# Performance work log

Measured on AMD Instinct MI355X. Metric: run time of the kernel, lower is better.

Reference implementation:

```python
import jax, jax.numpy as jnp
import numpy as np
import math

N_LEVELS = 16
F_PER = 2
LOG2T = 19
TABLE = 1 << LOG2T  # 524288
BASE = 16
FINEST = 512
BANDS = 10
TIME = 0.0

_B = math.exp((math.log(FINEST) - math.log(BASE)) / (N_LEVELS - 1))
_RES = [min(int(BASE * _B ** l), FINEST) for l in range(N_LEVELS)]
# primes reduced mod table size: (c*p) mod M == (c*(p mod M)) mod M, keeps products in int32 range
_PRIMES_MOD = np.array([73856093 % TABLE, 19349663 % TABLE, 83492791 % TABLE], dtype=np.int32)
_OFFSETS = np.array([[dx, dy, dz] for dx in (0, 1) for dy in (0, 1) for dz in (0, 1)], dtype=bool)  # [8,3]


def _hash_encode(x, tables):
    # x: [N,3] in [0,1]; tables: [L, 2^19, 2]
    x = jnp.clip(x, 0.0, 1.0)
    offs = jnp.asarray(_OFFSETS)[:, None, :]  # [8,1,3]
    pm = jnp.asarray(_PRIMES_MOD)
    outs = []
    for l in range(N_LEVELS):
        res = _RES[l]
        sc = x * (res - 1)                                   # [N,3]
        cf = jnp.clip(jnp.floor(sc).astype(jnp.int32), 0, res - 1)
        cc = jnp.clip(cf + 1, 0, res - 1)
        w = sc - cf.astype(sc.dtype)                         # trilinear weights [N,3]
        corner = jnp.where(offs, cc[None], cf[None])         # [8,N,3]
        h = ((corner[..., 0] * pm[0]) % TABLE
             + (corner[..., 1] * pm[1]) % TABLE
             + (corner[..., 2] * pm[2]) % TABLE) % TABLE     # [8,N]
        feats = tables[l][h]                                 # gather [8,N,2]
        cw = jnp.prod(jnp.where(offs, w[None], 1.0 - w[None]), axis=-1)  # [8,N]
        outs.append(jnp.sum(feats * cw[..., None], axis=0))  # [N,2]
    return jnp.concatenate(outs, axis=1)                     # [N,32]


def _freq_encode(freq):
    nf = (jnp.log10(jnp.clip(freq, 1e6, 1e12)) - 6.0) / 6.0  # [N,1]
    parts = []
    for i in range(BANDS):
        a = (2.0 ** i) * math.pi * nf
        parts += [jnp.sin(a), jnp.cos(a)]
    return jnp.concatenate(parts, axis=-1)                   # [N,20]


def _ln(x, g, b, eps=1e-5):
    m = jnp.mean(x, -1, keepdims=True)
    v = jnp.var(x, -1, keepdims=True)
    return (x - m) / jnp.sqrt(v + eps) * g + b


def _forward(x, frequency, tables, W0, b0, W1, b1, W2, b2, W3, b3,
             e_w1, e_b1, e_g, e_be, e_w2, e_b2,
             m_w1, m_b1, m_g, m_be, m_w2, m_b2,
             p_w1, p_b1, p_w2, p_b2,
             mat_w1, mat_b1, mat_w2, mat_b2,
             s_w1, s_b1, s_w2, s_b2):
    pe = _hash_encode(x, tables)                             # [N,32]
    fe = _freq_encode(frequency)                             # [N,20]
    feat0 = jnp.concatenate([pe, fe], axis=1)                # [N,52]
    h = jax.nn.relu(feat0 @ W0 + b0)
    h = jax.nn.relu(h @ W1 + b1)
    h = jax.nn.relu(jnp.concatenate([h, feat0], axis=1) @ W2 + b2)  # skip connection
    h = jax.nn.relu(h @ W3 + b3)
    E_amp = jnp.tanh(jax.nn.relu(_ln(h @ e_w1 + e_b1, e_g, e_be)) @ e_w2 + e_b2)
    B_amp = jnp.tanh(jax.nn.relu(_ln(h @ m_w1 + m_b1, m_g, m_be)) @ m_w2 + m_b2)
    phases = jax.nn.relu(h @ p_w1 + p_b1) @ p_w2 + p_b2      # [N,6]
    mat = jax.nn.relu(h @ mat_w1 + mat_b1) @ mat_w2 + mat_b2 # [N,3]
    src = jax.nn.relu(h @ s_w1 + s_b1) @ s_w2 + s_b2         # [N,4]
    omega = 2.0 * math.pi * frequency                        # [N,1]
    E = E_amp * jnp.cos(omega * TIME + phases[:, :3])
    B = B_amp * jnp.cos(omega * TIME + phases[:, 3:])
    eps_r = 1.0 + jax.nn.sigmoid(mat[:, 0:1]) * 10.0
    mu_r = 1.0 + jax.nn.sigmoid(mat[:, 1:2]) * 2.0
    cond = jax.nn.sigmoid(mat[:, 2:3]) * 0.01
    # pack all float outputs: E(3) B(3) eps(1) mu(1) cond(1) charge(1) current(3)
    return jnp.concatenate([E, B, eps_r, mu_r, cond, src[:, 0:1], src[:, 1:4]], axis=1)


def _lin_init(k, fan_in, fan_out):
    k1, k2 = jax.random.split(k)
    s = 1.0 / math.sqrt(fan_in)
    W = jax.random.uniform(k1, (fan_in, fan_out), jnp.float32, -s, s)
    b = jax.random.uniform(k2, (fan_out,), jnp.float32, -s, s)
    return W, b


def setup_inputs() -> dict:
    key = jax.random.key(0)
    ks = jax.random.split(key, 20)
    N = 262144
    d = {}
    d['x'] = jax.random.uniform(ks[0], (N, 3), jnp.float32)
    d['frequency'] = 10.0 ** jax.random.uniform(ks[1], (N, 1), jnp.float32, minval=6.0, maxval=12.0)
    d['tables'] = jax.random.normal(ks[2], (N_LEVELS, TABLE, F_PER), jnp.float32) * 1e-4
    layers = [('W0', 'b0', 52, 128), ('W1', 'b1', 128, 128), ('W2', 'b2', 180, 128), ('W3', 'b3', 128, 128),
              ('e_w1', 'e_b1', 128, 64), ('e_w2', 'e_b2', 64, 3),
              ('m_w1', 'm_b1', 128, 64), ('m_w2', 'm_b2', 64, 3),
              ('p_w1', 'p_b1', 128, 32), ('p_w2', 'p_b2', 32, 6),
              ('mat_w1', 'mat_b1', 128, 64), ('mat_w2', 'mat_b2', 64, 3),
              ('s_w1', 's_b1', 128, 64), ('s_w2', 's_b2', 64, 4)]
    for j, (wn, bn, fi, fo) in enumerate(layers):
        W, b = _lin_init(jax.random.fold_in(ks[3], j), fi, fo)
        d[wn] = W
        d[bn] = b
    d['e_g'] = jnp.ones(64, jnp.float32)
    d['e_be'] = jnp.zeros(64, jnp.float32)
    d['m_g'] = jnp.ones(64, jnp.float32)
    d['m_be'] = jnp.zeros(64, jnp.float32)
    return d


def reference(x, frequency, tables, W0, b0, W1, b1, W2, b2, W3, b3,
              e_w1, e_b1, e_g, e_be, e_w2, e_b2,
              m_w1, m_b1, m_g, m_be, m_w2, m_b2,
              p_w1, p_b1, p_w2, p_b2,
              mat_w1, mat_b1, mat_w2, mat_b2,
              s_w1, s_b1, s_w2, s_b2):
    return _forward(x, frequency, tables, W0, b0, W1, b1, W2, b2, W3, b3,
                    e_w1, e_b1, e_g, e_be, e_w2, e_b2,
                    m_w1, m_b1, m_g, m_be, m_w2, m_b2,
                    p_w1, p_b1, p_w2, p_b2,
                    mat_w1, mat_b1, mat_w2, mat_b2,
                    s_w1, s_b1, s_w2, s_b2)
```

## Files before the change

kernel.cpp:

```cpp
#include <hip/hip_runtime.h>
#include <math.h>

#define TMASK 524287
#define PM0 455773
#define PM1 475295
#define PM2 130999

typedef __attribute__((ext_vector_type(8))) short bf16x8;
typedef __attribute__((ext_vector_type(4))) float f32x4;

#define OFF_W0   0
#define OFF_W1   8192
#define OFF_W2   24576
#define OFF_W3   49152
#define OFF_E    65536
#define OFF_P    81920
#define OFF_MAT  86016
#define OFF_S    94208
#define OFF_BD   102400
#define WT_TOTAL 102400
#define WT_ALLOC 111616

#define WS_TAB8_OFF (WT_ALLOC*2)
#define TAB8_BYTES  (16u*524288u*2u)
#define WS_FEAT_OFF (WS_TAB8_OFF + TAB8_BYTES)
#define DENSE_BYTES 120992

#define TAB_SCALE   131072.0f
#define TAB_INV     (1.0f/131072.0f)

#define A6_H    0
#define A6_HL   8704
#define A6_FB   8704
#define LDS6_TOTAL 17408

struct Params {
  const float* x; const float* freq; const float* tables;
  const float* b0; const float* b1; const float* b2; const float* b3;
  const float* e_b1; const float* e_w2; const float* e_b2; const float* e_g; const float* e_be;
  const float* m_b1; const float* m_w2; const float* m_b2; const float* m_g; const float* m_be;
  const float* p_b1; const float* p_w2; const float* p_b2;
  const float* mat_b1; const float* mat_w2; const float* mat_b2;
  const float* s_b1; const float* s_w2; const float* s_b2;
  const short* wt;
  const unsigned* feat;
  const unsigned short* dense;
  float* out;
  int N;
  int res[16];
};

struct HashParams {
  const float* x; const unsigned short* tab8; unsigned* feat; int N; int res[16];
};
struct DensePrepParams { const unsigned short* tab8; unsigned short* dense; };
struct TabPrepParams { const float* tables; unsigned* tab8; };
struct PrepParams {
  const float* src[9];
  int end[9]; int Nsrc[9]; int Ksrc[9]; int Kpad[9];
  short* wt;
};
struct BdParams {
  const float* e; const float* m; const float* p; const float* mat; const float* s;
  short* out;
};

__device__ __forceinline__ short f2bf(float f){
  union { float f; unsigned u; } v; v.f = f;
  unsigned r = v.u + 0x7fffu + ((v.u >> 16) & 1u);
  return (short)(r >> 16);
}
__device__ __forceinline__ float bf2f(short s){
  union { unsigned u; float f; } v; v.u = ((unsigned)(unsigned short)s) << 16; return v.f;
}
__device__ __forceinline__ float sigmoid_(float v){ return 1.f/(1.f + expf(-v)); }

__global__ __launch_bounds__(256)
void prep_weights(PrepParams P)
{
  int id = blockIdx.x*256 + threadIdx.x;
  if (id >= WT_TOTAL) return;
  int r = 0, base = 0;
  #pragma unroll
  for (int i = 0; i < 9; ++i) { if (id >= P.end[i]) { r = i+1; base = P.end[i]; } }
  const int rel = id - base;
  const int kp = P.Kpad[r];
  const int n = rel / kp;
  const int k = rel - n*kp;
  float v = 0.f;
  if (k < P.Ksrc[r]) v = P.src[r][k * P.Nsrc[r] + n];
  P.wt[id] = f2bf(v);
}

__global__ __launch_bounds__(256)
void prep_bd(BdParams P)
{
  int id = blockIdx.x*256 + threadIdx.x;
  if (id >= 32*288) return;
  const int n = id / 288, k = id - n*288;
  float v = 0.f;
  if      (n < 3  && k < 64)                        v = P.e[k*3 + n];
  else if (n >= 3 && n < 6  && k >= 64  && k < 128) v = P.m[(k-64)*3 + (n-3)];
  else if (n >= 6 && n < 12 && k >= 256)            v = P.p[(k-256)*6 + (n-6)];
  else if (n >= 12&& n < 15 && k >= 128 && k < 192) v = P.mat[(k-128)*3 + (n-12)];
  else if (n >= 15&& n < 19 && k >= 192 && k < 256) v = P.s[(k-192)*4 + (n-15)];
  P.out[id] = f2bf(v);
}

__global__ __launch_bounds__(256)
void tab_prep(TabPrepParams P)
{
  const unsigned id = blockIdx.x*256 + threadIdx.x;
  if (id >= 16u*524288u/2u) return;
  const float4 v = ((const float4*)P.tables)[id];
  int q0 = (int)fminf(fmaxf(rintf(v.x*TAB_SCALE), -127.f), 127.f);
  int q1 = (int)fminf(fmaxf(rintf(v.y*TAB_SCALE), -127.f), 127.f);
  int q2 = (int)fminf(fmaxf(rintf(v.z*TAB_SCALE), -127.f), 127.f);
  int q3 = (int)fminf(fmaxf(rintf(v.w*TAB_SCALE), -127.f), 127.f);
  unsigned pack = (q0 & 255) | ((q1 & 255) << 8) | ((q2 & 255) << 16) | ((q3 & 255) << 24);
  P.tab8[id] = pack;
}

__global__ __launch_bounds__(256)
void dense_prep(DensePrepParams P)
{
  const int id = blockIdx.x*256 + threadIdx.x;
  const int l = id >> 15;
  const int c = id & 32767;
  const int RT4[4] = {16,20,25,32};
  const unsigned DOFFU[4] = {0, 4096, 12096, 27728};
  const int res = RT4[l];
  if (c >= res*res*res) return;
  const int cz = c % res;
  const int t  = c / res;
  const int cy = t % res;
  const int cx = t / res;
  const unsigned h = (unsigned)((cx*PM0 + cy*PM1 + cz*PM2) & TMASK);
  P.dense[DOFFU[l] + c] = P.tab8[((unsigned)l << 19) + h];
}

__global__ __launch_bounds__(256, 8)
void hash_encode12(HashParams P)
{
  const int b = blockIdx.x;
  const int unit = b % 24;
  const int strip = b / 24;
  const int l = 4 + (unit >> 1);
  const int half = unit & 1;
  const int halfN = (P.N + 1) >> 1;
  const int plA = strip*512 + threadIdx.x;
  if (plA >= halfN) return;
  const int plB = plA + 256;
  const bool vB = plB < halfN;
  int pA = half*halfN + plA;
  int pB = half*halfN + (vB ? plB : plA);
  const bool sA = pA < P.N;
  const bool sB = vB && (pB < P.N);
  if (pA >= P.N) pA = P.N - 1;
  if (pB >= P.N) pB = P.N - 1;

  const int res = P.res[l];
  const float rf = (float)(res-1);
  const unsigned short* tp = P.tab8 + ((size_t)l << 19);

  const float xA0 = fminf(fmaxf(P.x[pA*3+0], 0.f), 1.f);
  const float xA1 = fminf(fmaxf(P.x[pA*3+1], 0.f), 1.f);
  const float xA2 = fminf(fmaxf(P.x[pA*3+2], 0.f), 1.f);
  const float sA0 = xA0*rf, sA1 = xA1*rf, sA2 = xA2*rf;
  int fA0 = (int)sA0; if (fA0 > res-1) fA0 = res-1;
  int fA1 = (int)sA1; if (fA1 > res-1) fA1 = res-1;
  int fA2 = (int)sA2; if (fA2 > res-1) fA2 = res-1;
  const float wA0 = sA0 - (float)fA0;
  const float wA1 = sA1 - (float)fA1;
  const float wA2 = sA2 - (float)fA2;
  int cA0 = fA0+1; if (cA0 > res-1) cA0 = res-1;
  int cA1 = fA1+1; if (cA1 > res-1) cA1 = res-1;
  int cA2 = fA2+1; if (cA2 > res-1) cA2 = res-1;
  const int hxA0 = (fA0*PM0) & TMASK, hxA1 = (cA0*PM0) & TMASK;
  const int hyA0 = (fA1*PM1) & TMASK, hyA1 = (cA1*PM1) & TMASK;
  const int hzA0 = (fA2*PM2) & TMASK, hzA1 = (cA2*PM2) & TMASK;

  const float xB0 = fminf(fmaxf(P.x[pB*3+0], 0.f), 1.f);
  const float xB1 = fminf(fmaxf(P.x[pB*3+1], 0.f), 1.f);
  const float xB2 = fminf(fmaxf(P.x[pB*3+2], 0.f), 1.f);
  const float sB0 = xB0*rf, sB1 = xB1*rf, sB2 = xB2*rf;
  int fB0 = (int)sB0; if (fB0 > res-1) fB0 = res-1;
  int fB1 = (int)sB1; if (fB1 > res-1) fB1 = res-1;
  int fB2 = (int)sB2; if (fB2 > res-1) fB2 = res-1;
  const float wB0 = sB0 - (float)fB0;
  const float wB1 = sB1 - (float)fB1;
  const float wB2 = sB2 - (float)fB2;
  int cB0 = fB0+1; if (cB0 > res-1) cB0 = res-1;
  int cB1 = fB1+1; if (cB1 > res-1) cB1 = res-1;
  int cB2 = fB2+1; if (cB2 > res-1) cB2 = res-1;
  const int hxB0 = (fB0*PM0) & TMASK, hxB1 = (cB0*PM0) & TMASK;
  const int hyB0 = (fB1*PM1) & TMASK, hyB1 = (cB1*PM1) & TMASK;
  const int hzB0 = (fB2*PM2) & TMASK, hzB1 = (cB2*PM2) & TMASK;

  unsigned short tvA[8], tvB[8];
  #pragma unroll
  for (int cn = 0; cn < 8; ++cn) {
    const int bx = (cn>>2)&1, by = (cn>>1)&1, bz = cn&1;
    tvA[cn] = tp[((bx?hxA1:hxA0) + (by?hyA1:hyA0) + (bz?hzA1:hzA0)) & TMASK];
    tvB[cn] = tp[((bx?hxB1:hxB0) + (by?hyB1:hyB0) + (bz?hzB1:hzB0)) & TMASK];
  }

  unsigned* fl = P.feat + (size_t)(l-4)*P.N;
  {
    float a0 = 0.f, a1 = 0.f;
    #pragma unroll
    for (int cn = 0; cn < 8; ++cn) {
      const int bx = (cn>>2)&1, by = (cn>>1)&1, bz = cn&1;
      const float cw = (bx?wA0:1.f-wA0)*(by?wA1:1.f-wA1)*(bz?wA2:1.f-wA2);
      a0 = fmaf(cw, (float)(int)(signed char)(tvA[cn] & 0xff), a0);
      a1 = fmaf(cw, (float)(int)(signed char)(tvA[cn] >> 8),   a1);
    }
    a0 *= TAB_INV; a1 *= TAB_INV;
    if (sA)
      fl[pA] = (unsigned)(unsigned short)f2bf(a0)
             | ((unsigned)(unsigned short)f2bf(a1) << 16);
  }
  {
    float a0 = 0.f, a1 = 0.f;
    #pragma unroll
    for (int cn = 0; cn < 8; ++cn) {
      const int bx = (cn>>2)&1, by = (cn>>1)&1, bz = cn&1;
      const float cw = (bx?wB0:1.f-wB0)*(by?wB1:1.f-wB1)*(bz?wB2:1.f-wB2);
      a0 = fmaf(cw, (float)(int)(signed char)(tvB[cn] & 0xff), a0);
      a1 = fmaf(cw, (float)(int)(signed char)(tvB[cn] >> 8),   a1);
    }
    a0 *= TAB_INV; a1 *= TAB_INV;
    if (sB)
      fl[pB] = (unsigned)(unsigned short)f2bf(a0)
             | ((unsigned)(unsigned short)f2bf(a1) << 16);
  }
}

template<int NT, int KC>
__device__ __forceinline__ void gemm32(f32x4* acc0, f32x4* acc1,
    const short* A, int lda, const short* __restrict__ wt, int kpad, int kwoff,
    int n0, int q)
{
  const short* Ap0 = A + n0*lda + q*8;
  const short* Ap1 = Ap0 + 16*lda;
  const short* Bp  = wt + n0*kpad + kwoff + q*8;
  bf16x8 bc[NT], bn[NT];
  #pragma unroll
  for (int nt = 0; nt < NT; ++nt) bc[nt] = *(const bf16x8*)(Bp + nt*16*kpad);
  #pragma unroll
  for (int kc = 0; kc < KC; ++kc) {
    if (kc + 1 < KC) {
      #pragma unroll
      for (int nt = 0; nt < NT; ++nt)
        bn[nt] = *(const bf16x8*)(Bp + nt*16*kpad + (kc+1)*32);
    }
    const bf16x8 a0 = *(const bf16x8*)(Ap0 + kc*32);
    const bf16x8 a1 = *(const bf16x8*)(Ap1 + kc*32);
    #pragma unroll
    for (int nt = 0; nt < NT; ++nt) {
      acc0[nt] = __builtin_amdgcn_mfma_f32_16x16x32_bf16(a0, bc[nt], acc0[nt], 0, 0, 0);
      acc1[nt] = __builtin_amdgcn_mfma_f32_16x16x32_bf16(a1, bc[nt], acc1[nt], 0, 0, 0);
    }
    #pragma unroll
    for (int nt = 0; nt < NT; ++nt) bc[nt] = bn[nt];
  }
}

template<int NT>
__device__ __forceinline__ void epi_trunk(const f32x4* acc0, const f32x4* acc1,
    const float* bv4, short* out, int ldo, int n0, int q, int coff)
{
  #pragma unroll
  for (int nt = 0; nt < NT; ++nt) {
    const float bv = bv4[nt];
    #pragma unroll
    for (int r = 0; r < 4; ++r) {
      float v0 = fmaxf(acc0[nt][r] + bv, 0.f);
      float v1 = fmaxf(acc1[nt][r] + bv, 0.f);
      out[(q*4 + r)*ldo + coff + nt*16 + n0]      = f2bf(v0);
      out[(16 + q*4 + r)*ldo + coff + nt*16 + n0] = f2bf(v1);
    }
  }
}

__global__ __launch_bounds__(128, 4)
void em_nerf6(Params P)
{
  __shared__ __align__(16) char smem[LDS6_TOTAL];
  const int tid = threadIdx.x;
  const int lane = tid & 63, wave = tid >> 6;
  short* H  = (short*)(smem + A6_H);
  short* HL = (short*)(smem + A6_HL);
  short* FB = (short*)(smem + A6_FB);
  float* R2 = (float*)(smem + A6_HL);
  const int n0 = lane & 15, q = lane >> 4;
  const int p0 = blockIdx.x*32;
  const int ntb = wave*64;

  const int pp = tid & 31;
  const int lg = tid >> 5;

  unsigned fw3[3];
  {
    int gp = p0 + pp; if (gp >= P.N) gp = P.N - 1;
    #pragma unroll
    for (int j = 0; j < 3; ++j)
      fw3[j] = P.feat[(size_t)(lg*3 + j)*P.N + gp];
  }

  float rb0[4], rb1[4], rb2[4], rb3[4], rbem[4], rbms[4], rg[4], rbe[4];
  {
    const float* embp = wave ? P.m_b1 : P.e_b1;
    const float* msbp = wave ? P.s_b1 : P.mat_b1;
    const float* ggp  = wave ? P.m_g  : P.e_g;
    const float* bbep = wave ? P.m_be : P.e_be;
    #pragma unroll
    for (int nt = 0; nt < 4; ++nt) {
      const int c  = ntb + nt*16 + n0;
      const int ch = nt*16 + n0;
      rb0[nt] = P.b0[c]; rb1[nt] = P.b1[c]; rb2[nt] = P.b2[c]; rb3[nt] = P.b3[c];
      rbem[nt] = embp[ch]; rbms[nt] = msbp[ch];
      rg[nt] = ggp[ch]; rbe[nt] = bbep[ch];
    }
  }
  const float rpb = P.p_b1[wave*16 + n0];
  float rc;
  if (wave == 0) {
    if      (n0 < 3)  rc = P.e_b2[n0];
    else if (n0 < 6)  rc = P.m_b2[n0-3];
    else if (n0 < 12) rc = P.p_b2[n0-6];
    else if (n0 < 15) rc = P.mat_b2[n0-12];
    else              rc = P.s_b2[0];
  } else {
    rc = (n0 < 3) ? P.s_b2[1 + n0] : 0.f;
  }

  unsigned short ctv[8];
  float cw0, cw1, cw2;
  {
    int gpc = p0 + pp; if (gpc >= P.N) gpc = P.N - 1;
    const float xs0 = fminf(fmaxf(P.x[gpc*3+0], 0.f), 1.f);
    const float xs1 = fminf(fmaxf(P.x[gpc*3+1], 0.f), 1.f);
    const float xs2 = fminf(fmaxf(P.x[gpc*3+2], 0.f), 1.f);
    const int lo  = (lg & 1) ? 20 : 16;
    const int hi  = (lg & 1) ? 32 : 25;
    const int res = (lg & 2) ? hi : lo;
    const unsigned dlo  = (lg & 1) ? 4096u  : 0u;
    const unsigned dhi  = (lg & 1) ? 27728u : 12096u;
    const unsigned doff = (lg & 2) ? dhi : dlo;
    const float rf = (float)(res-1);
    const float s0 = xs0*rf, s1 = xs1*rf, s2 = xs2*rf;
    int f0i = (int)s0; if (f0i > res-1) f0i = res-1;
    int f1i = (int)s1; if (f1i > res-1) f1i = res-1;
    int f2i = (int)s2; if (f2i > res-1) f2i = res-1;
    cw0 = s0 - (float)f0i;
    cw1 = s1 - (float)f1i;
    cw2 = s2 - (float)f2i;
    int c0i = f0i+1; if (c0i > res-1) c0i = res-1;
    int c1i = f1i+1; if (c1i > res-1) c1i = res-1;
    int c2i = f2i+1; if (c2i > res-1) c2i = res-1;
    const int sx0 = f0i*res*res, sx1 = c0i*res*res;
    const int ty0 = f1i*res,     ty1 = c1i*res;
    const unsigned short* dp = P.dense + doff;
    #pragma unroll
    for (int cn = 0; cn < 8; ++cn) {
      const int bx = (cn>>2)&1, by = (cn>>1)&1, bz = cn&1;
      const int idx = (bx?sx1:sx0) + (by?ty1:ty0) + (bz?c2i:f2i);
      ctv[cn] = dp[idx];
    }
  }

  {
    int gp = p0 + pp; if (gp >= P.N) gp = P.N - 1;
    float fr = P.freq[gp];
    fr = fminf(fmaxf(fr, 1e6f), 1e12f);
    const float nf = (log10f(fr) - 6.f) * (1.f/6.f);
    const float a0 = 3.14159274101257324f * nf;
    #pragma clang loop unroll(disable)
    for (int i = lg; i < 10; i += 4) {
      const float a = a0 * (float)(1 << i);
      FB[pp*72 + 32 + 2*i] = f2bf(sinf(a));
      FB[pp*72 + 33 + 2*i] = f2bf(cosf(a));
    }
    if (lg == 3) {
      #pragma unroll
      for (int k = 52; k < 64; ++k) FB[pp*72 + k] = 0;
    }
  }

  {
    float a0 = 0.f, a1 = 0.f;
    #pragma unroll
    for (int cn = 0; cn < 8; ++cn) {
      const int bx = (cn>>2)&1, by = (cn>>1)&1, bz = cn&1;
      const float cw = (bx?cw0:1.f-cw0)*(by?cw1:1.f-cw1)*(bz?cw2:1.f-cw2);
      a0 = fmaf(cw, (float)(int)(signed char)(ctv[cn] & 0xff), a0);
      a1 = fmaf(cw, (float)(int)(signed char)(ctv[cn] >> 8),   a1);
    }
    a0 *= TAB_INV; a1 *= TAB_INV;
    const unsigned pack = (unsigned)(unsigned short)f2bf(a0)
                        | ((unsigned)(unsigned short)f2bf(a1) << 16);
    *(unsigned*)&FB[pp*72 + 2*lg] = pack;
  }

  #pragma unroll
  for (int j = 0; j < 3; ++j)
    *(unsigned*)&FB[pp*72 + 8 + 2*(lg*3 + j)] = fw3[j];
  __syncthreads();

  { f32x4 a0[4] = {}, a1[4] = {};
    gemm32<4,2>(a0, a1, FB, 72, P.wt + OFF_W0 + ntb*64, 64, 0, n0, q);
    epi_trunk<4>(a0, a1, rb0, H, 136, n0, q, ntb);
    __syncthreads(); }
  { f32x4 a0[4] = {}, a1[4] = {};
    gemm32<4,4>(a0, a1, H, 136, P.wt + OFF_W1 + ntb*128, 128, 0, n0, q);
    __syncthreads();
    epi_trunk<4>(a0, a1, rb1, H, 136, n0, q, ntb);
    __syncthreads(); }
  { f32x4 a0[4] = {}, a1[4] = {};
    gemm32<4,4>(a0, a1, H, 136, P.wt + OFF_W2 + ntb*192, 192, 0, n0, q);
    gemm32<4,2>(a0, a1, FB, 72, P.wt + OFF_W2 + ntb*192, 192, 128, n0, q);
    __syncthreads();
    epi_trunk<4>(a0, a1, rb2, H, 136, n0, q, ntb);
    __syncthreads(); }
  { f32x4 a0[4] = {}, a1[4] = {};
    gemm32<4,4>(a0, a1, H, 136, P.wt + OFF_W3 + ntb*128, 128, 0, n0, q);
    __syncthreads();
    epi_trunk<4>(a0, a1, rb3, H, 136, n0, q, ntb);
    __syncthreads(); }

  { f32x4 a0[4] = {}, a1[4] = {};
    gemm32<4,4>(a0, a1, H, 136, P.wt + OFF_E + ntb*128, 128, 0, n0, q);
    #pragma unroll
    for (int nt = 0; nt < 4; ++nt) {
      const float bv = rbem[nt];
      #pragma unroll
      for (int r = 0; r < 4; ++r) { a0[nt][r] += bv; a1[nt][r] += bv; }
    }
    float mn[2][4], iv[2][4];
    #pragma unroll
    for (int s = 0; s < 2; ++s) {
      const f32x4* A_ = s ? a1 : a0;
      #pragma unroll
      for (int r = 0; r < 4; ++r) {
        float se = 0.f, qe = 0.f;
        #pragma unroll
        for (int t = 0; t < 4; ++t) { const float x = A_[t][r]; se += x; qe = fmaf(x,x,qe); }
        #pragma unroll
        for (int msk = 1; msk < 16; msk <<= 1) {
          se += __shfl_xor(se, msk, 64);
          qe += __shfl_xor(qe, msk, 64);
        }
        const float me = se*(1.f/64.f);
        mn[s][r] = me;
        iv[s][r] = 1.f / sqrtf(qe*(1.f/64.f) - me*me + 1e-5f);
      }
    }
    #pragma unroll
    for (int t = 0; t < 4; ++t) {
      const float g  = rg[t];
      const float be = rbe[t];
      const int col = ntb + t*16 + n0;
      #pragma unroll
      for (int s = 0; s < 2; ++s) {
        const f32x4* A_ = s ? a1 : a0;
        #pragma unroll
        for (int r = 0; r < 4; ++r) {
          float v = (A_[t][r] - mn[s][r])*iv[s][r]*g + be;
          v = fmaxf(v, 0.f);
          HL[(s*16 + q*4 + r)*136 + col] = f2bf(v);
        }
      }
    }
  }
  __syncthreads();

  f32x4 o0[1] = {}, o1[1] = {};
  gemm32<1,4>(o0, o1, HL, 136, P.wt + OFF_BD + wave*16*288, 288, 0, n0, q);

  { f32x4 a0[4] = {}, a1[4] = {};
    gemm32<4,4>(a0, a1, H, 136, P.wt + OFF_MAT + ntb*128, 128, 0, n0, q);
    __syncthreads();
    #pragma unroll
    for (int t = 0; t < 4; ++t) {
      const float bv = rbms[t];
      const int col = ntb + t*16 + n0;
      #pragma unroll
      for (int s = 0; s < 2; ++s) {
        const f32x4* A_ = s ? a1 : a0;
        #pragma unroll
        for (int r = 0; r < 4; ++r)
          HL[(s*16 + q*4 + r)*136 + col] = f2bf(fmaxf(A_[t][r] + bv, 0.f));
      }
    }
  }
  __syncthreads();

  gemm32<1,4>(o0, o1, HL, 136, P.wt + OFF_BD + wave*16*288, 288, 128, n0, q);

  { f32x4 a0[1] = {}, a1[1] = {};
    gemm32<1,4>(a0, a1, H, 136, P.wt + OFF_P + wave*16*128, 128, 0, n0, q);
    __syncthreads();
    const int col = wave*16 + n0;
    #pragma unroll
    for (int s = 0; s < 2; ++s) {
      const f32x4* A_ = s ? a1 : a0;
      #pragma unroll
      for (int r = 0; r < 4; ++r)
        HL[(s*16 + q*4 + r)*136 + col] = f2bf(fmaxf(A_[0][r] + rpb, 0.f));
    }
  }
  __syncthreads();

  gemm32<1,1>(o0, o1, HL, 136, P.wt + OFF_BD + wave*16*288, 288, 256, n0, q);
  __syncthreads();

  #pragma unroll
  for (int s = 0; s < 2; ++s) {
    const f32x4* O_ = s ? o1 : o0;
    #pragma unroll
    for (int r = 0; r < 4; ++r) {
      const int p = s*16 + q*4 + r;
      if (wave == 0) {
        float v0 = O_[0][r] + rc;
        if (n0 < 6) v0 = tanhf(v0);
        R2[p*20 + n0] = v0;
      } else if (n0 < 3) {
        R2[p*20 + 16 + n0] = O_[0][r] + rc;
      }
    }
  }
  __syncthreads();

  if (tid < 32) {
    const int gp = p0 + tid;
    if (gp < P.N) {
      const float* r = R2 + tid*20;
      float* o = P.out + (size_t)gp*13;
      o[0] = r[0]*cosf(r[6]);
      o[1] = r[1]*cosf(r[7]);
      o[2] = r[2]*cosf(r[8]);
      o[3] = r[3]*cosf(r[9]);
      o[4] = r[4]*cosf(r[10]);
      o[5] = r[5]*cosf(r[11]);
      o[6] = 1.f + sigmoid_(r[12])*10.f;
      o[7] = 1.f + sigmoid_(r[13])*2.f;
      o[8] = sigmoid_(r[14])*0.01f;
      o[9]  = r[15];
      o[10] = r[16];
      o[11] = r[17];
      o[12] = r[18];
    }
  }
}

__global__ __launch_bounds__(256, 3)
void em_nerf_fallback(Params P)
{
  __shared__ __align__(16) char smem[44288];
  short* featB = (short*)smem;
  short* hA    = (short*)(smem + 9216);
  short* hB    = (short*)(smem + 9216 + 17664);
  float* headF = (float*)(smem + 9216);
  float* res2  = (float*)smem;
  __shared__ int s_res[16];

  const int tid = threadIdx.x;
  if (tid < 16) s_res[tid] = P.res[tid];
  __syncthreads();
  {
    const int p = tid & 63;
    const int g = tid >> 6;
    int gp = blockIdx.x*64 + p; if (gp >= P.N) gp = P.N - 1;
    const float xs0 = fminf(fmaxf(P.x[gp*3+0], 0.f), 1.f);
    const float xs1 = fminf(fmaxf(P.x[gp*3+1], 0.f), 1.f);
    const float xs2 = fminf(fmaxf(P.x[gp*3+2], 0.f), 1.f);
    #pragma unroll
    for (int j = 0; j < 4; ++j) {
      const int l = g*4 + j;
      const int res = s_res[l];
      const float rf = (float)(res-1);
      const float s0 = xs0*rf, s1 = xs1*rf, s2 = xs2*rf;
      int f0i = (int)s0; if (f0i > res-1) f0i = res-1;
      int f1i = (int)s1; if (f1i > res-1) f1i = res-1;
      int f2i = (int)s2; if (f2i > res-1) f2i = res-1;
      const float w0 = s0 - (float)f0i;
      const float w1 = s1 - (float)f1i;
      const float w2 = s2 - (float)f2i;
      int c0i = f0i+1; if (c0i > res-1) c0i = res-1;
      int c1i = f1i+1; if (c1i > res-1) c1i = res-1;
      int c2i = f2i+1; if (c2i > res-1) c2i = res-1;
      const int hx0 = (f0i*PM0) & TMASK, hx1 = (c0i*PM0) & TMASK;
      const int hy0 = (f1i*PM1) & TMASK, hy1 = (c1i*PM1) & TMASK;
      const int hz0 = (f2i*PM2) & TMASK, hz1 = (c2i*PM2) & TMASK;
      const float* tp = P.tables + ((size_t)l << 20);
      float a0 = 0.f, a1 = 0.f;
      #pragma unroll
      for (int cn = 0; cn < 8; ++cn) {
        const int bx = (cn>>2)&1, by = (cn>>1)&1, bz = cn&1;
        const int hh = ((bx?hx1:hx0) + (by?hy1:hy0) + (bz?hz1:hz0)) & TMASK;
        const float cw = (bx?w0:1.f-w0)*(by?w1:1.f-w1)*(bz?w2:1.f-w2);
        const float2 tv = *(const float2*)(tp + 2*hh);
        a0 = fmaf(cw, tv.x, a0);
        a1 = fmaf(cw, tv.y, a1);
      }
      featB[p*72 + 2*l]   = f2bf(a0);
      featB[p*72 + 2*l+1] = f2bf(a1);
    }
    if (g == 0) {
      float fr = P.freq[gp];
      fr = fminf(fmaxf(fr, 1e6f), 1e12f);
      const float nf = (log10f(fr) - 6.f) * (1.f/6.f);
      float a = 3.14159274101257324f * nf;
      #pragma unroll
      for (int i = 0; i < 10; ++i) {
        featB[p*72 + 32 + 2*i] = f2bf(sinf(a));
        featB[p*72 + 33 + 2*i] = f2bf(cosf(a));
        a = a * 2.f;
      }
    }
    if (g == 3) {
      #pragma unroll
      for (int k = 52; k < 64; ++k) featB[p*72 + k] = 0;
    }
  }
  __syncthreads();

  const int lane = tid & 63, wave = tid >> 6;
  const int n0 = lane & 15, q = lane >> 4;
  short* myA  = featB + wave*16*72;
  short* myH1 = hA + wave*16*136;
  short* myH2 = hB + wave*16*136;

  auto gemm1 = [&](const short* A, int lda, const short* wt, int kpad, int kwoff, int KC, f32x4* acc, int NT){
    const short* Ap = A + n0*lda + q*8;
    const short* Bp = wt + n0*kpad + kwoff + q*8;
    for (int kc = 0; kc < KC; ++kc) {
      bf16x8 a = *(const bf16x8*)(Ap + kc*32);
      for (int nt = 0; nt < NT; ++nt) {
        bf16x8 b = *(const bf16x8*)(Bp + nt*16*kpad + kc*32);
        acc[nt] = __builtin_amdgcn_mfma_f32_16x16x32_bf16(a, b, acc[nt], 0, 0, 0);
      }
    }
  };
  auto epi1 = [&](const f32x4* acc, const float* bias, short* out, int ldo, int NT, bool relu){
    for (int nt = 0; nt < NT; ++nt) {
      const float bv = bias[nt*16 + n0];
      for (int r = 0; r < 4; ++r) {
        float v = acc[nt][r] + bv;
        if (relu) v = fmaxf(v, 0.f);
        out[(q*4 + r)*ldo + nt*16 + n0] = f2bf(v);
      }
    }
  };

  { f32x4 acc[8] = {}; gemm1(myA, 72, P.wt + OFF_W0, 64, 0, 2, acc, 8);  epi1(acc, P.b0, myH1, 136, 8, true); }
  __syncthreads();
  { f32x4 acc[8] = {}; gemm1(myH1, 136, P.wt + OFF_W1, 128, 0, 4, acc, 8); epi1(acc, P.b1, myH2, 136, 8, true); }
  __syncthreads();
  { f32x4 acc[8] = {}; gemm1(myH2, 136, P.wt + OFF_W2, 192, 0, 4, acc, 8);
    gemm1(myA, 72, P.wt + OFF_W2, 192, 128, 2, acc, 8); epi1(acc, P.b2, myH1, 136, 8, true); }
  __syncthreads();
  { f32x4 acc[8] = {}; gemm1(myH1, 136, P.wt + OFF_W3, 128, 0, 4, acc, 8); epi1(acc, P.b3, myH2, 136, 8, true); }
  __syncthreads();

  float* hf = headF + wave*16*69;
  auto head1f = [&](const short* wt, const float* bias, int NT, bool relu){
    f32x4 acc[4] = {};
    gemm1(myH2, 136, wt, 128, 0, 4, acc, NT);
    for (int nt = 0; nt < NT; ++nt) {
      const float bv = bias[nt*16 + n0];
      for (int r = 0; r < 4; ++r) {
        float v = acc[nt][r] + bv;
        if (relu) v = fmaxf(v, 0.f);
        hf[(q*4 + r)*69 + nt*16 + n0] = v;
      }
    }
  };
  auto l2 = [&](int OC2, int K2, bool ln, bool th, const float* g, const float* be,
                const float* W2, const float* b2, int slot){
    __syncthreads();
    if (tid < 64) {
      const float* row = headF + tid*69;
      float mn = 0.f, iv = 1.f;
      if (ln) {
        float s = 0.f;
        for (int k = 0; k < K2; ++k) s += row[k];
        mn = s/(float)K2;
        float vv = 0.f;
        for (int k = 0; k < K2; ++k) { float d = row[k]-mn; vv = fmaf(d,d,vv); }
        iv = 1.f/sqrtf(vv/(float)K2 + 1e-5f);
      }
      for (int j = 0; j < OC2; ++j) {
        float acc = b2[j];
        for (int k = 0; k < K2; ++k) {
          float xv = row[k];
          if (ln) xv = (xv-mn)*iv*g[k] + be[k];
          xv = fmaxf(xv, 0.f);
          acc = fmaf(xv, W2[k*OC2+j], acc);
        }
        res2[tid*20 + slot + j] = th ? tanhf(acc) : acc;
      }
    }
    __syncthreads();
  };

  head1f(P.wt + OFF_E, P.e_b1, 4, false); l2(3, 64, true,  true,  P.e_g, P.e_be, P.e_w2, P.e_b2, 0);
  head1f(P.wt + OFF_E + 8192, P.m_b1, 4, false); l2(3, 64, true, true, P.m_g, P.m_be, P.m_w2, P.m_b2, 3);
  head1f(P.wt + OFF_P, P.p_b1, 2, true);  l2(6, 32, false, false, 0, 0, P.p_w2, P.p_b2, 6);
  head1f(P.wt + OFF_MAT, P.mat_b1, 4, true); l2(3, 64, false, false, 0, 0, P.mat_w2, P.mat_b2, 12);
  head1f(P.wt + OFF_S, P.s_b1, 4, true);  l2(4, 64, false, false, 0, 0, P.s_w2, P.s_b2, 15);

  if (tid < 64) {
    const int gp = blockIdx.x*64 + tid;
    if (gp < P.N) {
      const float* r = res2 + tid*20;
      float* o = P.out + (size_t)gp*13;
      o[0] = r[0]*cosf(r[6]);
      o[1] = r[1]*cosf(r[7]);
      o[2] = r[2]*cosf(r[8]);
      o[3] = r[3]*cosf(r[9]);
      o[4] = r[4]*cosf(r[10]);
      o[5] = r[5]*cosf(r[11]);
      o[6] = 1.f + sigmoid_(r[12])*10.f;
      o[7] = 1.f + sigmoid_(r[13])*2.f;
      o[8] = sigmoid_(r[14])*0.01f;
      o[9]  = r[15];
      o[10] = r[16];
      o[11] = r[17];
      o[12] = r[18];
    }
  }
}

extern "C" void kernel_launch(void* const* d_in, const int* in_sizes, int n_in,
                              void* d_out, int out_size, void* d_ws, size_t ws_size,
                              hipStream_t stream) {
  (void)n_in; (void)out_size;
  const float** in = (const float**)d_in;
  const int N = in_sizes[0] / 3;

  PrepParams PP;
  const float* srcs[9] = { in[3], in[5], in[7], in[9], in[11], in[15], in[19], in[23], in[27] };
  const int ends[9]  = { 8192, 24576, 49152, 65536, 73728, 81920, 86016, 94208, 102400 };
  const int nsrc[9]  = { 128, 128, 128, 128, 64, 64, 32, 64, 64 };
  const int ksrc[9]  = { 52, 128, 180, 128, 128, 128, 128, 128, 128 };
  const int kpad[9]  = { 64, 128, 192, 128, 128, 128, 128, 128, 128 };
  for (int i = 0; i < 9; ++i) { PP.src[i]=srcs[i]; PP.end[i]=ends[i]; PP.Nsrc[i]=nsrc[i]; PP.Ksrc[i]=ksrc[i]; PP.Kpad[i]=kpad[i]; }
  PP.wt = (short*)d_ws;
  hipLaunchKernelGGL(prep_weights, dim3((WT_TOTAL+255)/256), dim3(256), 0, stream, PP);

  BdParams BP;
  BP.e = in[13]; BP.m = in[17]; BP.p = in[21]; BP.mat = in[25]; BP.s = in[29];
  BP.out = (short*)d_ws + OFF_BD;
  hipLaunchKernelGGL(prep_bd, dim3((32*288 + 255)/256), dim3(256), 0, stream, BP);

  Params P;
  P.x = in[0]; P.freq = in[1]; P.tables = in[2];
  P.b0 = in[4]; P.b1 = in[6]; P.b2 = in[8]; P.b3 = in[10];
  P.e_b1 = in[12]; P.e_w2 = in[13]; P.e_b2 = in[14];
  P.m_b1 = in[16]; P.m_w2 = in[17]; P.m_b2 = in[18];
  P.p_b1 = in[20]; P.p_w2 = in[21]; P.p_b2 = in[22];
  P.mat_b1 = in[24]; P.mat_w2 = in[25]; P.mat_b2 = in[26];
  P.s_b1 = in[28]; P.s_w2 = in[29]; P.s_b2 = in[30];
  P.e_g = in[31]; P.e_be = in[32]; P.m_g = in[33]; P.m_be = in[34];
  P.wt = (const short*)d_ws;
  P.feat = (const unsigned*)((const char*)d_ws + WS_FEAT_OFF);
  P.out = (float*)d_out;
  P.N = N;

  const double B = exp((log(512.0) - log(16.0)) / 15.0);
  for (int l = 0; l < 16; ++l) {
    double r = 16.0 * pow(B, (double)l);
    int ri = (int)r;
    if (ri > 512) ri = 512;
    P.res[l] = ri;
  }

  const size_t feat_bytes = (size_t)N*12*4;
  const size_t need = (size_t)WS_FEAT_OFF + feat_bytes + DENSE_BYTES;

  if (ws_size >= need) {
    char* dense_base = (char*)d_ws + WS_FEAT_OFF + feat_bytes;
    P.dense = (const unsigned short*)dense_base;

    TabPrepParams TP;
    TP.tables = in[2];
    TP.tab8 = (unsigned*)((char*)d_ws + WS_TAB8_OFF);
    hipLaunchKernelGGL(tab_prep, dim3((16*524288/2 + 255)/256), dim3(256), 0, stream, TP);

    DensePrepParams DP;
    DP.tab8 = (const unsigned short*)((const char*)d_ws + WS_TAB8_OFF);
    DP.dense = (unsigned short*)dense_base;
    hipLaunchKernelGGL(dense_prep, dim3(4*32768/256), dim3(256), 0, stream, DP);

    HashParams HP;
    HP.x = in[0];
    HP.tab8 = (const unsigned short*)((const char*)d_ws + WS_TAB8_OFF);
    HP.feat = (unsigned*)((char*)d_ws + WS_FEAT_OFF);
    HP.N = N;
    for (int l = 0; l < 16; ++l) HP.res[l] = P.res[l];
    const int halfN = (N + 1) >> 1;
    const int strips = (halfN + 511) / 512;
    hipLaunchKernelGGL(hash_encode12, dim3(strips*24), dim3(256), 0, stream, HP);

    hipLaunchKernelGGL(em_nerf6, dim3((N + 31) / 32), dim3(128), 0, stream, P);
  } else {
    P.dense = nullptr;
    hipLaunchKernelGGL(em_nerf_fallback, dim3((N + 63) / 64), dim3(256), 0, stream, P);
  }
}
```

Baseline: 491.1 us.

## Extend dense-grid precompute to levels 4-7 and blend them in main kernel

Levels 4-7 get a dense pre-gathered grid, the same treatment levels 0-3 already had, so their lookups index a compact array instead of the scattered hash table. The main kernel now computes these mid levels inline, and the separate hash kernel handles only levels 8-15. This shrinks the intermediate feature buffer and the hash kernel's work. In exchange, the dense prep kernel must gather about a million entries per call, and the main kernel takes on eight more gathers per point.

After: 471.2 us. 1.04x faster.

```diff
diff --git a/kernel.cpp b/kernel.cpp
--- a/kernel.cpp
+++ b/kernel.cpp
@@ -24,7 +24,8 @@
 #define WS_TAB8_OFF (WT_ALLOC*2)
 #define TAB8_BYTES  (16u*524288u*2u)
 #define WS_FEAT_OFF (WS_TAB8_OFF + TAB8_BYTES)
-#define DENSE_BYTES 120992
+#define DENSE_USHORTS 1023640
+#define DENSE_BYTES   (DENSE_USHORTS*2)
 
 #define TAB_SCALE   131072.0f
 #define TAB_INV     (1.0f/131072.0f)
@@ -122,30 +123,35 @@
 }
 
 __global__ __launch_bounds__(256)
-void dense_prep(DensePrepParams P)
+void dense_prep8(DensePrepParams P)
 {
   const int id = blockIdx.x*256 + threadIdx.x;
-  const int l = id >> 15;
-  const int c = id & 32767;
-  const int RT4[4] = {16,20,25,32};
-  const unsigned DOFFU[4] = {0, 4096, 12096, 27728};
-  const int res = RT4[l];
+  if (id >= DENSE_USHORTS) return;
+  int l = 0, base = 0, res = 16;
+  if (id >= 4096)   { l = 1; base = 4096;   res = 20; }
+  if (id >= 12096)  { l = 2; base = 12096;  res = 25; }
+  if (id >= 27728)  { l = 3; base = 27728;  res = 32; }
+  if (id >= 60496)  { l = 4; base = 60496;  res = 40; }
+  if (id >= 124496) { l = 5; base = 124496; res = 50; }
+  if (id >= 249496) { l = 6; base = 249496; res = 64; }
+  if (id >= 511640) { l = 7; base = 511640; res = 80; }
+  const int c = id - base;
   if (c >= res*res*res) return;
   const int cz = c % res;
   const int t  = c / res;
   const int cy = t % res;
   const int cx = t / res;
   const unsigned h = (unsigned)((cx*PM0 + cy*PM1 + cz*PM2) & TMASK);
-  P.dense[DOFFU[l] + c] = P.tab8[((unsigned)l << 19) + h];
+  P.dense[id] = P.tab8[((unsigned)l << 19) + h];
 }
 
 __global__ __launch_bounds__(256, 8)
-void hash_encode12(HashParams P)
+void hash_encode8lv(HashParams P)
 {
   const int b = blockIdx.x;
-  const int unit = b % 24;
-  const int strip = b / 24;
-  const int l = 4 + (unit >> 1);
+  const int unit = b % 16;
+  const int strip = b / 16;
+  const int l = 8 + (unit >> 1);
   const int half = unit & 1;
   const int halfN = (P.N + 1) >> 1;
   const int plA = strip*512 + threadIdx.x;
@@ -205,7 +211,7 @@
     tvB[cn] = tp[((bx?hxB1:hxB0) + (by?hyB1:hyB0) + (bz?hzB1:hzB0)) & TMASK];
   }
 
-  unsigned* fl = P.feat + (size_t)(l-4)*P.N;
+  unsigned* fl = P.feat + (size_t)(l-8)*P.N;
   {
     float a0 = 0.f, a1 = 0.f;
     #pragma unroll
@@ -234,6 +240,42 @@
       fl[pB] = (unsigned)(unsigned short)f2bf(a0)
              | ((unsigned)(unsigned short)f2bf(a1) << 16);
   }
+}
+
+__device__ __forceinline__ unsigned dense_blend(
+    const unsigned short* __restrict__ dp, int res,
+    float xs0, float xs1, float xs2)
+{
+  const float rf = (float)(res-1);
+  const float s0 = xs0*rf, s1 = xs1*rf, s2 = xs2*rf;
+  int f0i = (int)s0; if (f0i > res-1) f0i = res-1;
+  int f1i = (int)s1; if (f1i > res-1) f1i = res-1;
+  int f2i = (int)s2; if (f2i > res-1) f2i = res-1;
+  const float w0 = s0 - (float)f0i;
+  const float w1 = s1 - (float)f1i;
+  const float w2 = s2 - (float)f2i;
+  int c0i = f0i+1; if (c0i > res-1) c0i = res-1;
+  int c1i = f1i+1; if (c1i > res-1) c1i = res-1;
+  int c2i = f2i+1; if (c2i > res-1) c2i = res-1;
+  const int sx0 = f0i*res*res, sx1 = c0i*res*res;
+  const int ty0 = f1i*res,     ty1 = c1i*res;
+  unsigned short tv[8];
+  #pragma unroll
+  for (int cn = 0; cn < 8; ++cn) {
+    const int bx = (cn>>2)&1, by = (cn>>1)&1, bz = cn&1;
+    tv[cn] = dp[(bx?sx1:sx0) + (by?ty1:ty0) + (bz?c2i:f2i)];
+  }
+  float a0 = 0.f, a1 = 0.f;
+  #pragma unroll
+  for (int cn = 0; cn < 8; ++cn) {
+    const int bx = (cn>>2)&1, by = (cn>>1)&1, bz = cn&1;
+    const float cw = (bx?w0:1.f-w0)*(by?w1:1.f-w1)*(bz?w2:1.f-w2);
+    a0 = fmaf(cw, (float)(int)(signed char)(tv[cn] & 0xff), a0);
+    a1 = fmaf(cw, (float)(int)(signed char)(tv[cn] >> 8),   a1);
+  }
+  a0 *= TAB_INV; a1 *= TAB_INV;
+  return (unsigned)(unsigned short)f2bf(a0)
+       | ((unsigned)(unsigned short)f2bf(a1) << 16);
 }
 
 template<int NT, int KC>
@@ -299,14 +341,16 @@
 
   const int pp = tid & 31;
   const int lg = tid >> 5;
-
-  unsigned fw3[3];
-  {
-    int gp = p0 + pp; if (gp >= P.N) gp = P.N - 1;
-    #pragma unroll
-    for (int j = 0; j < 3; ++j)
-      fw3[j] = P.feat[(size_t)(lg*3 + j)*P.N + gp];
-  }
+  int gp = p0 + pp; if (gp >= P.N) gp = P.N - 1;
+
+  unsigned fw2[2];
+  #pragma unroll
+  for (int j = 0; j < 2; ++j)
+    fw2[j] = P.feat[(size_t)(lg*2 + j)*P.N + gp];
+
+  const float xs0 = fminf(fmaxf(P.x[gp*3+0], 0.f), 1.f);
+  const float xs1 = fminf(fmaxf(P.x[gp*3+1], 0.f), 1.f);
+  const float xs2 = fminf(fmaxf(P.x[gp*3+2], 0.f), 1.f);
 
   float rb0[4], rb1[4], rb2[4], rb3[4], rbem[4], rbms[4], rg[4], rbe[4];
   {
@@ -335,43 +379,29 @@
     rc = (n0 < 3) ? P.s_b2[1 + n0] : 0.f;
   }
 
-  unsigned short ctv[8];
-  float cw0, cw1, cw2;
+  unsigned coarse_pack;
   {
-    int gpc = p0 + pp; if (gpc >= P.N) gpc = P.N - 1;
-    const float xs0 = fminf(fmaxf(P.x[gpc*3+0], 0.f), 1.f);
-    const float xs1 = fminf(fmaxf(P.x[gpc*3+1], 0.f), 1.f);
-    const float xs2 = fminf(fmaxf(P.x[gpc*3+2], 0.f), 1.f);
     const int lo  = (lg & 1) ? 20 : 16;
     const int hi  = (lg & 1) ? 32 : 25;
     const int res = (lg & 2) ? hi : lo;
     const unsigned dlo  = (lg & 1) ? 4096u  : 0u;
     const unsigned dhi  = (lg & 1) ? 27728u : 12096u;
     const unsigned doff = (lg & 2) ? dhi : dlo;
-    const float rf = (float)(res-1);
-    const float s0 = xs0*rf, s1 = xs1*rf, s2 = xs2*rf;
-    int f0i = (int)s0; if (f0i > res-1) f0i = res-1;
-    int f1i = (int)s1; if (f1i > res-1) f1i = res-1;
-    int f2i = (int)s2; if (f2i > res-1) f2i = res-1;
-    cw0 = s0 - (float)f0i;
-    cw1 = s1 - (float)f1i;
-    cw2 = s2 - (float)f2i;
-    int c0i = f0i+1; if (c0i > res-1) c0i = res-1;
-    int c1i = f1i+1; if (c1i > res-1) c1i = res-1;
-    int c2i = f2i+1; if (c2i > res-1) c2i = res-1;
-    const int sx0 = f0i*res*res, sx1 = c0i*res*res;
-    const int ty0 = f1i*res,     ty1 = c1i*res;
-    const unsigned short* dp = P.dense + doff;
-    #pragma unroll
-    for (int cn = 0; cn < 8; ++cn) {
-      const int bx = (cn>>2)&1, by = (cn>>1)&1, bz = cn&1;
-      const int idx = (bx?sx1:sx0) + (by?ty1:ty0) + (bz?c2i:f2i);
-      ctv[cn] = dp[idx];
-    }
-  }
-
+    coarse_pack = dense_blend(P.dense + doff, res, xs0, xs1, xs2);
+  }
+
+  unsigned mid_pack;
   {
-    int gp = p0 + pp; if (gp >= P.N) gp = P.N - 1;
+    const int lo  = (lg & 1) ? 50 : 40;
+    const int hi  = (lg & 1) ? 80 : 64;
+    const int res = (lg & 2) ? hi : lo;
+    const unsigned dlo  = (lg & 1) ? 124496u : 60496u;
+    const unsigned dhi  = (lg & 1) ? 511640u : 249496u;
+    const unsigned doff = (lg & 2) ? dhi : dlo;
+    mid_pack = dense_blend(P.dense + doff, res, xs0, xs1, xs2);
+  }
+
+  {
     float fr = P.freq[gp];
     fr = fminf(fmaxf(fr, 1e6f), 1e12f);
     const float nf = (log10f(fr) - 6.f) * (1.f/6.f);
@@ -388,24 +418,11 @@
     }
   }
 
-  {
-    float a0 = 0.f, a1 = 0.f;
-    #pragma unroll
-    for (int cn = 0; cn < 8; ++cn) {
-      const int bx = (cn>>2)&1, by = (cn>>1)&1, bz = cn&1;
-      const float cw = (bx?cw0:1.f-cw0)*(by?cw1:1.f-cw1)*(bz?cw2:1.f-cw2);
-      a0 = fmaf(cw, (float)(int)(signed char)(ctv[cn] & 0xff), a0);
-      a1 = fmaf(cw, (float)(int)(signed char)(ctv[cn] >> 8),   a1);
-    }
-    a0 *= TAB_INV; a1 *= TAB_INV;
-    const unsigned pack = (unsigned)(unsigned short)f2bf(a0)
-                        | ((unsigned)(unsigned short)f2bf(a1) << 16);
-    *(unsigned*)&FB[pp*72 + 2*lg] = pack;
-  }
-
-  #pragma unroll
-  for (int j = 0; j < 3; ++j)
-    *(unsigned*)&FB[pp*72 + 8 + 2*(lg*3 + j)] = fw3[j];
+  *(unsigned*)&FB[pp*72 + 2*lg] = coarse_pack;
+  *(unsigned*)&FB[pp*72 + 8 + 2*lg] = mid_pack;
+  #pragma unroll
+  for (int j = 0; j < 2; ++j)
+    *(unsigned*)&FB[pp*72 + 16 + 4*lg + 2*j] = fw2[j];
   __syncthreads();
 
   { f32x4 a0[4] = {}, a1[4] = {};
@@ -533,10 +550,10 @@
   __syncthreads();
 
   if (tid < 32) {
-    const int gp = p0 + tid;
-    if (gp < P.N) {
+    const int gp2 = p0 + tid;
+    if (gp2 < P.N) {
       const float* r = R2 + tid*20;
-      float* o = P.out + (size_t)gp*13;
+      float* o = P.out + (size_t)gp2*13;
       o[0] = r[0]*cosf(r[6]);
       o[1] = r[1]*cosf(r[7]);
       o[2] = r[2]*cosf(r[8]);
@@ -777,7 +794,7 @@
     P.res[l] = ri;
   }
 
-  const size_t feat_bytes = (size_t)N*12*4;
+  const size_t feat_bytes = (size_t)N*8*4;
   const size_t need = (size_t)WS_FEAT_OFF + feat_bytes + DENSE_BYTES;
 
   if (ws_size >= need) {
@@ -792,7 +809,7 @@
     DensePrepParams DP;
     DP.tab8 = (const unsigned short*)((const char*)d_ws + WS_TAB8_OFF);
     DP.dense = (unsigned short*)dense_base;
-    hipLaunchKernelGGL(dense_prep, dim3(4*32768/256), dim3(256), 0, stream, DP);
+    hipLaunchKernelGGL(dense_prep8, dim3((DENSE_USHORTS + 255)/256), dim3(256), 0, stream, DP);
 
     HashParams HP;
     HP.x = in[0];
@@ -802,7 +819,7 @@
     for (int l = 0; l < 16; ++l) HP.res[l] = P.res[l];
     const int halfN = (N + 1) >> 1;
     const int strips = (halfN + 511) / 512;
-    hipLaunchKernelGGL(hash_encode12, dim3(strips*24), dim3(256), 0, stream, HP);
+    hipLaunchKernelGGL(hash_encode8lv, dim3(strips*16), dim3(256), 0, stream, HP);
 
     hipLaunchKernelGGL(em_nerf6, dim3((N + 31) / 32), dim3(128), 0, stream, P);
   } else {
```
